# Kernel optimization log

Hardware: AMD Instinct MI355X
Metric: run time of the kernel (lower is better)

## Reference

```python
import jax, jax.numpy as jnp
import numpy as np

B, K, M, L = 16, 256, 16, 64
DET_C, HID, H, DEPTH = 1152, 128, 4, 2
DK = HID // H
SCALE = np.float32(1.0 / np.sqrt(DK))


def _ln(x, g, b):
    mu = jnp.mean(x, -1, keepdims=True)
    v = jnp.mean((x - mu) ** 2, -1, keepdims=True)
    return (x - mu) * jax.lax.rsqrt(v + 1e-5) * g + b


def _bn(x, g, b, m, v):  # eval-mode BatchNorm1d, channel-last
    return (x - m) * (g * jax.lax.rsqrt(v + 1e-5)) + b


def _prelu(x, a):
    return jnp.where(x >= 0, x, a * x)


def _mha(q_in, k_in, v_in, Wq, bq, Wk, bk, Wv, bv, Wo, bo, lg, lb, bias=None, mask=None):
    # MultiHeadAttention: scaled dot-product + residual + LayerNorm (eval, no dropout)
    Bb, Nq, _ = q_in.shape
    Nk = k_in.shape[1]
    q = (q_in @ Wq.T + bq).reshape(Bb, Nq, H, DK).transpose(0, 2, 1, 3)
    k = (k_in @ Wk.T + bk).reshape(Bb, Nk, H, DK).transpose(0, 2, 1, 3)
    v = (v_in @ Wv.T + bv).reshape(Bb, Nk, H, DK).transpose(0, 2, 1, 3)
    att = jnp.einsum('bhqd,bhkd->bhqk', q, k) * SCALE
    if bias is not None:
        att = att + bias  # way='add': per-head distance bias
    if mask is not None:
        att = jnp.where(mask, jnp.float32(-1e9), att)
    att = jax.nn.softmax(att, axis=-1)
    out = jnp.einsum('bhqk,bhkd->bhqd', att, v).transpose(0, 2, 1, 3).reshape(Bb, Nq, HID)
    out = out @ Wo.T + bo
    return _ln(q_in + out, lg, lb)


def setup_inputs() -> dict:
    key = jax.random.key(0)
    ks = iter(jax.random.split(key, 64))
    def nrm(shape, s=0.05):
        return jax.random.normal(next(ks), shape, jnp.float32) * s
    d = {}
    d['center'] = jax.random.normal(next(ks), (B, K, 3), jnp.float32)
    d['detr_features'] = nrm((B, K, DET_C), 1.0)
    d['lang_fea'] = nrm((B * M, L, HID), 1.0)
    d['fc_W1'] = nrm((HID, DET_C)); d['fc_b1'] = jnp.zeros((HID,), jnp.float32)
    for pre in ['bn1', 'mbn1', 'mbn2']:
        d[pre + '_g'] = jnp.ones((HID,), jnp.float32)
        d[pre + '_b'] = jnp.zeros((HID,), jnp.float32)
        d[pre + '_m'] = jnp.zeros((HID,), jnp.float32)
        d[pre + '_v'] = jnp.ones((HID,), jnp.float32)
    d['pr1_a'] = 0.25 * jnp.ones((HID,), jnp.float32)
    d['fc_W2'] = nrm((HID, HID)); d['fc_b2'] = jnp.zeros((HID,), jnp.float32)
    for pre in ['sa', 'ca']:
        for nm in ['Wq', 'Wk', 'Wv', 'Wo']:
            d[f'{pre}_{nm}'] = nrm((DEPTH, HID, HID))
        for nm in ['bq', 'bk', 'bv', 'bo', 'lb']:
            d[f'{pre}_{nm}'] = jnp.zeros((DEPTH, HID), jnp.float32)
        d[f'{pre}_lg'] = jnp.ones((DEPTH, HID), jnp.float32)
    d['m_W1'] = nrm((HID, HID)); d['m_b1'] = jnp.zeros((HID,), jnp.float32)
    d['mp1_a'] = 0.25 * jnp.ones((1,), jnp.float32)
    d['m_W2'] = nrm((HID, HID)); d['m_b2'] = jnp.zeros((HID,), jnp.float32)
    d['mp2_a'] = 0.25 * jnp.ones((1,), jnp.float32)
    d['m_W3'] = nrm((1, HID)); d['m_b3'] = jnp.zeros((1,), jnp.float32)
    d['attention_mask'] = jax.random.bernoulli(next(ks), 0.2, (B * M, 1, 1, L))
    d['len_nun_max'] = M
    return d


def reference(center, detr_features, lang_fea,
              fc_W1, fc_b1, bn1_g, bn1_b, bn1_m, bn1_v, pr1_a, fc_W2, fc_b2,
              sa_Wq, sa_bq, sa_Wk, sa_bk, sa_Wv, sa_bv, sa_Wo, sa_bo, sa_lg, sa_lb,
              ca_Wq, ca_bq, ca_Wk, ca_bk, ca_Wv, ca_bv, ca_Wo, ca_bo, ca_lg, ca_lb,
              m_W1, m_b1, mbn1_g, mbn1_b, mbn1_m, mbn1_v, mp1_a,
              m_W2, m_b2, mbn2_g, mbn2_b, mbn2_m, mbn2_v, mp2_a,
              m_W3, m_b3, attention_mask, len_nun_max):
    # distance-based attention bias (detached in the original)
    c = jax.lax.stop_gradient(center)
    dist = jnp.sqrt(jnp.sum((c[:, None, :, :] - c[:, :, None, :]) ** 2, -1))[:, None]  # (B,1,K,K)
    dw = 1.0 / (dist + 0.01)
    dw = dw / jnp.sum(dw, axis=2, keepdims=True)
    zeros = jnp.zeros_like(dw)
    dist_weights = jnp.concatenate([dw, -dist, zeros, zeros], axis=1)  # (B,H,K,K), one bias per head

    # features_concat: Conv1d(1x1) + BN + PReLU + Conv1d(1x1), channel-last
    x = detr_features @ fc_W1.T + fc_b1
    x = _prelu(_bn(x, bn1_g, bn1_b, bn1_m, bn1_v), pr1_a)
    x = x @ fc_W2.T + fc_b2  # (B,K,HID)

    feats = _mha(x, x, x, sa_Wq[0], sa_bq[0], sa_Wk[0], sa_bk[0], sa_Wv[0], sa_bv[0],
                 sa_Wo[0], sa_bo[0], sa_lg[0], sa_lb[0], bias=dist_weights)

    m = int(len_nun_max)
    feats = jnp.broadcast_to(feats[:, None], (B, m, K, HID)).reshape(B * m, K, HID)
    dwb = jnp.broadcast_to(dist_weights[:, None], (B, m, H, K, K)).reshape(B * m, H, K, K)

    f1 = _mha(feats, lang_fea, lang_fea, ca_Wq[0], ca_bq[0], ca_Wk[0], ca_bk[0], ca_Wv[0],
              ca_bv[0], ca_Wo[0], ca_bo[0], ca_lg[0], ca_lb[0], mask=attention_mask)
    for i in range(1, DEPTH):
        f1 = _mha(f1, f1, f1, sa_Wq[i], sa_bq[i], sa_Wk[i], sa_bk[i], sa_Wv[i], sa_bv[i],
                  sa_Wo[i], sa_bo[i], sa_lg[i], sa_lb[i], bias=dwb)
        f1 = _mha(f1, lang_fea, lang_fea, ca_Wq[i], ca_bq[i], ca_Wk[i], ca_bk[i], ca_Wv[i],
                  ca_bv[i], ca_Wo[i], ca_bo[i], ca_lg[i], ca_lb[i], mask=attention_mask)

    # match head: conv1x1+BN+PReLU x2 + conv1x1 -> 1
    y = f1 @ m_W1.T + m_b1
    y = _prelu(_bn(y, mbn1_g, mbn1_b, mbn1_m, mbn1_v), mp1_a)
    y = y @ m_W2.T + m_b2
    y = _prelu(_bn(y, mbn2_g, mbn2_b, mbn2_m, mbn2_v), mp2_a)
    conf = (y @ m_W3.T + m_b3)[..., 0]  # (B*M, K) cluster_ref
    return conf
```

## Files before the change

kernel.cpp:

```cpp
#include <hip/hip_runtime.h>
#include <hip/hip_bf16.h>
#include <cstdio>

#define KQ   256
#define HID  128
typedef unsigned short u16;
#define SCALE_F 0.1767766952966369f

typedef __bf16 bf16x8 __attribute__((ext_vector_type(8)));
typedef short  s16x8  __attribute__((ext_vector_type(8)));
typedef float  f32x4  __attribute__((ext_vector_type(4)));

static __device__ __forceinline__ float bfu(u16 u) {
    return __uint_as_float(((unsigned)u) << 16);
}
static __device__ __forceinline__ u16 f2b(float f) {
    unsigned u = __float_as_uint(f);
    return (u16)((u + 0x7FFFu + ((u >> 16) & 1u)) >> 16);
}
static __device__ __forceinline__ float ldf(const void* p, int i, int f) {
    return f ? ((const float*)p)[i] : bfu(((const u16*)p)[i]);
}
static __device__ __forceinline__ f32x4 mfma16(s16x8 a, s16x8 b, f32x4 c) {
    return __builtin_amdgcn_mfma_f32_16x16x32_bf16(
        __builtin_bit_cast(bf16x8, a), __builtin_bit_cast(bf16x8, b), c, 0, 0, 0);
}

#define OFF_WB     8256
#define OFF_LANGB  237632
#define OFF_DWB    1286208
#define OFF_DIST   2334784
#define OFF_ROWS   3383360
#define OFF_FEATSB 3387456
#define OFF_FAB    3649600
#define OFF_QB     7843904
#define OFF_KB     12038208
#define OFF_VB     16232512
#define OFF_MASK   20426816
#define NEEDF      20430912

#define WB_FCW1 0
#define WB_FCW2 147456
#define WB_SAWQ 163840
#define WB_SAWK 196608
#define WB_SAWV 229376
#define WB_SAWO 262144
#define WB_CAWQ 294912
#define WB_CAWK 327680
#define WB_CAWV 360448
#define WB_CAWO 393216
#define WB_MW1  425984
#define WB_MW2  442368

__global__ __launch_bounds__(256) void k_detect(
    const unsigned* __restrict__ onesw, const unsigned* __restrict__ maskw,
    int* __restrict__ flags)
{
    __shared__ int fb;
    if (threadIdx.x == 0) fb = 0;
    __syncthreads();
    int any = 0;
    for (int i = threadIdx.x; i < 4096; i += 256) any |= (maskw[i] > 1u) ? 1 : 0;
    if (any) atomicOr(&fb, 1);
    __syncthreads();
    if (threadIdx.x == 0) {
        flags[0] = (onesw[0] == 0x3F800000u) ? 1 : 0;
        flags[1] = fb;
    }
}

__global__ __launch_bounds__(256) void k_mask_canon(
    const unsigned char* __restrict__ raw, const int* __restrict__ flags,
    unsigned char* __restrict__ mask8)
{
    int i = blockIdx.x*256 + threadIdx.x;
    if (flags[1]) mask8[i] = raw[i] ? 1 : 0;
    else          mask8[i] = (((const unsigned int*)raw)[i] != 0u) ? 1 : 0;
}

__global__ __launch_bounds__(256) void k_cv16(
    const void* __restrict__ src, u16* __restrict__ dst, int n,
    const int* __restrict__ flags)
{
    int i = (blockIdx.x*256 + threadIdx.x)*4;
    if (i >= n) return;
    if (flags[0]) {
        float4 v = *(const float4*)((const float*)src + i);
        ushort4 o; o.x = f2b(v.x); o.y = f2b(v.y); o.z = f2b(v.z); o.w = f2b(v.w);
        *(ushort4*)(dst + i) = o;
    } else {
        *(ushort4*)(dst + i) = *(const ushort4*)((const u16*)src + i);
    }
}

__global__ __launch_bounds__(256) void k_dist(
    const void* __restrict__ center, float* __restrict__ dist,
    float* __restrict__ dwraw, float* __restrict__ rowsum,
    const int* __restrict__ flags)
{
    int f  = flags[0];
    int bi = blockIdx.x, b = bi >> 8, j = threadIdx.x;
    float cx = ldf(center, bi*3+0, f), cy = ldf(center, bi*3+1, f), cz = ldf(center, bi*3+2, f);
    int pj = (b << 8) + j;
    float px = ldf(center, pj*3+0, f), py = ldf(center, pj*3+1, f), pz = ldf(center, pj*3+2, f);
    float dx = px-cx, dy = py-cy, dz = pz-cz;
    float d  = sqrtf(dx*dx + dy*dy + dz*dz);
    float w  = 1.f/(d + 0.01f);
    int o = bi*256 + j;
    dist[o]  = d;
    dwraw[o] = w;
    float sw = w;
    #pragma unroll
    for (int m = 32; m >= 1; m >>= 1) sw += __shfl_xor(sw, m);
    __shared__ float red[4];
    if ((j & 63) == 0) red[j >> 6] = sw;
    __syncthreads();
    if (j == 0) rowsum[bi] = red[0] + red[1] + red[2] + red[3];
}

__global__ __launch_bounds__(256) void k_dwnorm(
    float* __restrict__ dw, const float* __restrict__ rowsum)
{
    int i = blockIdx.x*256 + threadIdx.x;
    int b = i >> 16, kc = i & 255;
    dw[i] = dw[i] / rowsum[(b << 8) + kc];
}

template<int EPI, bool ABCAST, bool RBCAST>
__global__ __launch_bounds__(256) void k_gemm(
    const u16* __restrict__ A, const u16* __restrict__ W, u16* __restrict__ C,
    int Kd, const void* __restrict__ bias,
    const void* __restrict__ bng, const void* __restrict__ bnb,
    const void* __restrict__ bnm, const void* __restrict__ bnv,
    const void* __restrict__ pa,
    const void* __restrict__ lg, const void* __restrict__ lb,
    const u16* __restrict__ resid, const int* __restrict__ flags, int voff)
{
    __shared__ __align__(16) u16 Wl[128*136];
    int f = flags[0];
    int t = threadIdx.x, w = t>>6, lane = t&63, lm = lane&15, q4 = lane>>4;
    int m0 = blockIdx.x*64;
    int arow = m0 + w*16 + lm;
    int grow = ABCAST ? (((arow>>12)<<8)|(arow&255)) : arow;
    const u16* Abase = A + (size_t)grow*Kd;
    f32x4 acc[8];
    #pragma unroll
    for (int nt = 0; nt < 8; ++nt) acc[nt] = f32x4{0.f,0.f,0.f,0.f};
    int sr = t>>1, ss = (t&1)*64;
    for (int k0 = 0; k0 < Kd; k0 += 128) {
        const u16* src = W + (size_t)sr*Kd + k0 + ss;
        u16* dst = Wl + sr*136 + ss;
        #pragma unroll
        for (int i = 0; i < 8; ++i) *(s16x8*)(dst + i*8) = *(const s16x8*)(src + i*8);
        __syncthreads();
        s16x8 aF[4];
        #pragma unroll
        for (int ks = 0; ks < 4; ++ks) aF[ks] = *(const s16x8*)(Abase + k0 + ks*32 + q4*8);
        #pragma unroll
        for (int nt = 0; nt < 8; ++nt)
            #pragma unroll
            for (int ks = 0; ks < 4; ++ks) {
                s16x8 bF = *(const s16x8*)(Wl + (nt*16+lm)*136 + ks*32 + q4*8);
                acc[nt] = mfma16(aF[ks], bF, acc[nt]);
            }
        __syncthreads();
    }
    int row = m0 + w*16 + q4*4;
    if (EPI == 3) {
        float xs[8][4];
        #pragma unroll
        for (int nt = 0; nt < 8; ++nt) {
            int ch = nt*16 + lm;
            float bs = ldf(bias, voff + ch, f);
            #pragma unroll
            for (int r = 0; r < 4; ++r) {
                int rr = row + r;
                int rrow = RBCAST ? (((rr>>12)<<8)|(rr&255)) : rr;
                xs[nt][r] = acc[nt][r] + bs + bfu(resid[(size_t)rrow*HID + ch]);
            }
        }
        #pragma unroll
        for (int r = 0; r < 4; ++r) {
            float sm = 0.f, sq = 0.f;
            #pragma unroll
            for (int nt = 0; nt < 8; ++nt) { sm += xs[nt][r]; sq += xs[nt][r]*xs[nt][r]; }
            #pragma unroll
            for (int d = 1; d <= 8; d <<= 1) { sm += __shfl_xor(sm, d); sq += __shfl_xor(sq, d); }
            float mean = sm * (1.f/128.f);
            float var  = sq * (1.f/128.f) - mean*mean;
            float rs   = rsqrtf(var + 1e-5f);
            #pragma unroll
            for (int nt = 0; nt < 8; ++nt) {
                int ch = nt*16 + lm;
                float g = ldf(lg, voff + ch, f), bb = ldf(lb, voff + ch, f);
                C[(size_t)(row+r)*HID + ch] = f2b((xs[nt][r]-mean)*rs*g + bb);
            }
        }
    } else {
        #pragma unroll
        for (int nt = 0; nt < 8; ++nt) {
            int ch = nt*16 + lm;
            float bs = ldf(bias, voff + ch, f);
            float scl = 1.f, sh = 0.f, al = 0.f;
            if (EPI >= 1) {
                float g  = ldf(bng, ch, f), bb = ldf(bnb, ch, f);
                float mn = ldf(bnm, ch, f), vv = ldf(bnv, ch, f);
                scl = g * rsqrtf(vv + 1e-5f);
                sh  = bb - mn*scl;
                al  = (EPI == 2) ? ldf(pa, 0, f) : ldf(pa, ch, f);
            }
            #pragma unroll
            for (int r = 0; r < 4; ++r) {
                float x = acc[nt][r] + bs;
                if (EPI >= 1) { x = x*scl + sh; x = (x >= 0.f) ? x : al*x; }
                C[(size_t)(row+r)*HID + ch] = f2b(x);
            }
        }
    }
}

template<int NK, int MODE>
__global__ __launch_bounds__(256) void k_attn_m(
    const u16* __restrict__ Q, const u16* __restrict__ K, const u16* __restrict__ V,
    u16* __restrict__ O, const float* __restrict__ dwb, const float* __restrict__ dist,
    const unsigned char* __restrict__ mask, int bdiv)
{
    constexpr int NKP = NK + 8;
    __shared__ __align__(16) u16 Vt[32*NKP];
    __shared__ __align__(16) u16 P[4][16*NKP];
    int s = blockIdx.x, h = blockIdx.y, qt = blockIdx.z;
    int t = threadIdx.x, w = t>>6, lane = t&63, lm = lane&15, q4 = lane>>4;
    for (int idx = t; idx < NK*8; idx += 256) {
        int k = idx >> 3, d4 = idx & 7;
        ushort4 u = *(const ushort4*)(V + ((size_t)s*NK + k)*HID + h*32 + d4*4);
        Vt[(d4*4+0)*NKP + k] = u.x;
        Vt[(d4*4+1)*NKP + k] = u.y;
        Vt[(d4*4+2)*NKP + k] = u.z;
        Vt[(d4*4+3)*NKP + k] = u.w;
    }
    __syncthreads();
    int qrow0 = qt*64 + w*16;
    s16x8 aq = *(const s16x8*)(Q + ((size_t)s*KQ + qrow0 + lm)*HID + h*32 + q4*8);
    float S[NK/16][4];
    const float* bp = nullptr; float bsgn = 1.f;
    if (MODE == 1) { if (h == 0) bp = dwb; else if (h == 1) { bp = dist; bsgn = -1.f; } }
    int qb = (MODE == 1) ? ((s/bdiv)*256) : 0;
    #pragma unroll
    for (int kt = 0; kt < NK/16; ++kt) {
        s16x8 bk = *(const s16x8*)(K + ((size_t)s*NK + kt*16 + lm)*HID + h*32 + q4*8);
        f32x4 acc = f32x4{0.f,0.f,0.f,0.f};
        acc = mfma16(aq, bk, acc);
        int key = kt*16 + lm;
        float madd = 0.f;
        if (MODE == 0) madd = mask[s*NK + key] ? -1.0e9f : 0.f;
        #pragma unroll
        for (int r = 0; r < 4; ++r) {
            float sc = acc[r]*SCALE_F;
            if (MODE == 1) { if (bp) sc += bsgn*bp[(size_t)(qb + qrow0 + q4*4 + r)*256 + key]; }
            else sc += madd;
            S[kt][r] = sc;
        }
    }
    float l[4];
    #pragma unroll
    for (int r = 0; r < 4; ++r) {
        float m = -3.0e38f;
        #pragma unroll
        for (int kt = 0; kt < NK/16; ++kt) m = fmaxf(m, S[kt][r]);
        #pragma unroll
        for (int d = 1; d <= 8; d <<= 1) m = fmaxf(m, __shfl_xor(m, d));
        float sum = 0.f;
        #pragma unroll
        for (int kt = 0; kt < NK/16; ++kt) { float p = __expf(S[kt][r]-m); S[kt][r] = p; sum += p; }
        #pragma unroll
        for (int d = 1; d <= 8; d <<= 1) sum += __shfl_xor(sum, d);
        l[r] = sum;
    }
    u16* Pw = P[w];
    #pragma unroll
    for (int kt = 0; kt < NK/16; ++kt)
        #pragma unroll
        for (int r = 0; r < 4; ++r)
            Pw[(q4*4+r)*NKP + kt*16 + lm] = f2b(S[kt][r]);
    __syncthreads();
    #pragma unroll
    for (int nt = 0; nt < 2; ++nt) {
        f32x4 acc = f32x4{0.f,0.f,0.f,0.f};
        #pragma unroll
        for (int ks = 0; ks < NK/32; ++ks) {
            s16x8 ap = *(const s16x8*)(Pw + lm*NKP + ks*32 + q4*8);
            s16x8 bv = *(const s16x8*)(Vt + (nt*16+lm)*NKP + ks*32 + q4*8);
            acc = mfma16(ap, bv, acc);
        }
        #pragma unroll
        for (int r = 0; r < 4; ++r)
            O[((size_t)s*KQ + qrow0 + q4*4 + r)*HID + h*32 + nt*16 + lm] = f2b(acc[r] / l[r]);
    }
}

__global__ __launch_bounds__(256) void k_final(
    const u16* __restrict__ Y, const void* __restrict__ w3,
    const void* __restrict__ b3, void* __restrict__ outp,
    const int* __restrict__ flags)
{
    int f = flags[0];
    int w = threadIdx.x >> 6, lane = threadIdx.x & 63;
    int row = blockIdx.x*4 + w;
    float p = bfu(Y[(size_t)row*HID + lane])*ldf(w3, lane, f)
            + bfu(Y[(size_t)row*HID + 64 + lane])*ldf(w3, 64+lane, f);
    #pragma unroll
    for (int m = 32; m >= 1; m >>= 1) p += __shfl_xor(p, m);
    if (lane == 0) {
        float r = p + ldf(b3, 0, f);
        if (f) ((float*)outp)[row] = r;
        else   ((u16*)outp)[row]   = f2b(r);
    }
}

extern "C" void kernel_launch(void* const* d_in, const int* in_sizes, int n_in,
                              void* d_out, int out_size, void* d_ws, size_t ws_size,
                              hipStream_t stream)
{
    (void)n_in;
    if (ws_size < (size_t)NEEDF * 4) {
        fprintf(stderr, "kernel_launch: ws too small: have %zu need %zu\n",
                ws_size, (size_t)NEEDF * 4);
        hipMemsetAsync(d_out, 0, (size_t)out_size * 2, stream);
        return;
    }
    float* F = (float*)d_ws;
    u16*   U = (u16*)d_ws;
    int* flags = (int*)d_ws;
    u16* WB     = U + (size_t)OFF_WB*2;
    u16* langb  = U + (size_t)OFF_LANGB*2;
    u16* detrb  = U + (size_t)OFF_KB*2;
    u16* featsb = U + (size_t)OFF_FEATSB*2;
    u16* x2b    = U + (size_t)OFF_FAB*2;
    u16* fAb    = U + (size_t)OFF_FAB*2;
    u16* x1b    = U + (size_t)OFF_VB*2;
    u16* Qb     = U + (size_t)OFF_QB*2;
    u16* Kb     = U + (size_t)OFF_KB*2;
    u16* Vb     = U + (size_t)OFF_VB*2;
    float* dwb    = F + OFF_DWB;
    float* dist   = F + OFF_DIST;
    float* rowsum = F + OFF_ROWS;
    unsigned char* mask8 = (unsigned char*)(F + OFF_MASK);

    k_detect<<<1, 256, 0, stream>>>((const unsigned*)d_in[8],
                                    (const unsigned*)d_in[48], flags);
    k_mask_canon<<<64, 256, 0, stream>>>((const unsigned char*)d_in[48], flags, mask8);

    struct { int idx; u16* dst; int n; } cv[14] = {
        {3,  WB+WB_FCW1, 147456}, {18, WB+WB_FCW2, 16384},
        {20, WB+WB_SAWQ, 32768}, {21, WB+WB_SAWK, 32768},
        {22, WB+WB_SAWV, 32768}, {23, WB+WB_SAWO, 32768},
        {30, WB+WB_CAWQ, 32768}, {31, WB+WB_CAWK, 32768},
        {32, WB+WB_CAWV, 32768}, {33, WB+WB_CAWO, 32768},
        {40, WB+WB_MW1, 16384},  {43, WB+WB_MW2, 16384},
        {1,  detrb, 4718592},    {2,  langb, 2097152},
    };
    for (int e = 0; e < 14; ++e)
        k_cv16<<<(cv[e].n + 1023)/1024, 256, 0, stream>>>(
            d_in[cv[e].idx], cv[e].dst, cv[e].n, flags);

    k_dist<<<4096, 256, 0, stream>>>(d_in[0], dist, dwb, rowsum, flags);
    k_dwnorm<<<4096, 256, 0, stream>>>(dwb, rowsum);

    const void* N0 = nullptr;

    k_gemm<1,false,false><<<64, 256, 0, stream>>>(detrb, WB+WB_FCW1, x1b, 1152,
        d_in[4], d_in[5], d_in[6], d_in[7], d_in[8], d_in[17], N0, N0, nullptr, flags, 0);
    k_gemm<0,false,false><<<64, 256, 0, stream>>>(x1b, WB+WB_FCW2, x2b, 128,
        d_in[19], N0,N0,N0,N0,N0, N0, N0, nullptr, flags, 0);

    k_gemm<0,false,false><<<64, 256, 0, stream>>>(x2b, WB+WB_SAWQ, Qb, 128,
        d_in[24], N0,N0,N0,N0,N0, N0, N0, nullptr, flags, 0);
    k_gemm<0,false,false><<<64, 256, 0, stream>>>(x2b, WB+WB_SAWK, Kb, 128,
        d_in[25], N0,N0,N0,N0,N0, N0, N0, nullptr, flags, 0);
    k_gemm<0,false,false><<<64, 256, 0, stream>>>(x2b, WB+WB_SAWV, Vb, 128,
        d_in[26], N0,N0,N0,N0,N0, N0, N0, nullptr, flags, 0);
    k_attn_m<256,1><<<dim3(16,4,4), 256, 0, stream>>>(Qb, Kb, Vb, Qb, dwb, dist, nullptr, 1);
    k_gemm<3,false,false><<<64, 256, 0, stream>>>(Qb, WB+WB_SAWO, featsb, 128,
        d_in[27], N0,N0,N0,N0,N0, d_in[29], d_in[28], x2b, flags, 0);

    k_gemm<0,true, false><<<1024, 256, 0, stream>>>(featsb, WB+WB_CAWQ, Qb, 128,
        d_in[34], N0,N0,N0,N0,N0, N0, N0, nullptr, flags, 0);
    k_gemm<0,false,false><<<256,  256, 0, stream>>>(langb, WB+WB_CAWK, Kb, 128,
        d_in[35], N0,N0,N0,N0,N0, N0, N0, nullptr, flags, 0);
    k_gemm<0,false,false><<<256,  256, 0, stream>>>(langb, WB+WB_CAWV, Vb, 128,
        d_in[36], N0,N0,N0,N0,N0, N0, N0, nullptr, flags, 0);
    k_attn_m<64,0><<<dim3(256,4,4), 256, 0, stream>>>(Qb, Kb, Vb, Qb, nullptr, nullptr, mask8, 1);
    k_gemm<3,false,true><<<1024, 256, 0, stream>>>(Qb, WB+WB_CAWO, fAb, 128,
        d_in[37], N0,N0,N0,N0,N0, d_in[39], d_in[38], featsb, flags, 0);

    k_gemm<0,false,false><<<1024, 256, 0, stream>>>(fAb, WB+WB_SAWQ+16384, Qb, 128,
        d_in[24], N0,N0,N0,N0,N0, N0, N0, nullptr, flags, 128);
    k_gemm<0,false,false><<<1024, 256, 0, stream>>>(fAb, WB+WB_SAWK+16384, Kb, 128,
        d_in[25], N0,N0,N0,N0,N0, N0, N0, nullptr, flags, 128);
    k_gemm<0,false,false><<<1024, 256, 0, stream>>>(fAb, WB+WB_SAWV+16384, Vb, 128,
        d_in[26], N0,N0,N0,N0,N0, N0, N0, nullptr, flags, 128);
    k_attn_m<256,1><<<dim3(256,4,4), 256, 0, stream>>>(Qb, Kb, Vb, Qb, dwb, dist, nullptr, 16);
    k_gemm<3,false,false><<<1024, 256, 0, stream>>>(Qb, WB+WB_SAWO+16384, fAb, 128,
        d_in[27], N0,N0,N0,N0,N0, d_in[29], d_in[28], fAb, flags, 128);

    k_gemm<0,false,false><<<1024, 256, 0, stream>>>(fAb, WB+WB_CAWQ+16384, Qb, 128,
        d_in[34], N0,N0,N0,N0,N0, N0, N0, nullptr, flags, 128);
    k_gemm<0,false,false><<<256,  256, 0, stream>>>(langb, WB+WB_CAWK+16384, Kb, 128,
        d_in[35], N0,N0,N0,N0,N0, N0, N0, nullptr, flags, 128);
    k_gemm<0,false,false><<<256,  256, 0, stream>>>(langb, WB+WB_CAWV+16384, Vb, 128,
        d_in[36], N0,N0,N0,N0,N0, N0, N0, nullptr, flags, 128);
    k_attn_m<64,0><<<dim3(256,4,4), 256, 0, stream>>>(Qb, Kb, Vb, Qb, nullptr, nullptr, mask8, 1);
    k_gemm<3,false,false><<<1024, 256, 0, stream>>>(Qb, WB+WB_CAWO+16384, fAb, 128,
        d_in[37], N0,N0,N0,N0,N0, d_in[39], d_in[38], fAb, flags, 128);

    k_gemm<2,false,false><<<1024, 256, 0, stream>>>(fAb, WB+WB_MW1, Qb, 128,
        d_in[41], d_in[9], d_in[10], d_in[11], d_in[12], d_in[42], N0, N0, nullptr, flags, 0);
    k_gemm<2,false,false><<<1024, 256, 0, stream>>>(Qb, WB+WB_MW2, Kb, 128,
        d_in[44], d_in[13], d_in[14], d_in[15], d_in[16], d_in[45], N0, N0, nullptr, flags, 0);
    k_final<<<16384, 256, 0, stream>>>(Kb, d_in[46], d_in[47], d_out, flags);
}
```

Measured before the change: 622.9 us.

## Recompute distance bias inside self-attention and stage K/V once per head block

Drops the materialised dist and normalized distance-weight matrices and their normalization kernel. Self-attention now recomputes pairwise distances from centers held in shared memory, keeping only a per-row sum buffer. Both attention kernels also loop over the four query tiles inside one block, so K and V for a head are staged in LDS once instead of per query tile. This cuts global traffic for the bias and the repeated K/V loads, at the cost of extra sqrt/div per score for two heads and a quarter as many blocks.

```diff
diff --git a/kernel.cpp b/kernel.cpp
--- a/kernel.cpp
+++ b/kernel.cpp
@@ -93,9 +93,8 @@
     }
 }
 
-__global__ __launch_bounds__(256) void k_dist(
-    const void* __restrict__ center, float* __restrict__ dist,
-    float* __restrict__ dwraw, float* __restrict__ rowsum,
+__global__ __launch_bounds__(256) void k_rowsum(
+    const void* __restrict__ center, float* __restrict__ rowsum,
     const int* __restrict__ flags)
 {
     int f  = flags[0];
@@ -106,9 +105,6 @@
     float dx = px-cx, dy = py-cy, dz = pz-cz;
     float d  = sqrtf(dx*dx + dy*dy + dz*dz);
     float w  = 1.f/(d + 0.01f);
-    int o = bi*256 + j;
-    dist[o]  = d;
-    dwraw[o] = w;
     float sw = w;
     #pragma unroll
     for (int m = 32; m >= 1; m >>= 1) sw += __shfl_xor(sw, m);
@@ -116,14 +112,6 @@
     if ((j & 63) == 0) red[j >> 6] = sw;
     __syncthreads();
     if (j == 0) rowsum[bi] = red[0] + red[1] + red[2] + red[3];
-}
-
-__global__ __launch_bounds__(256) void k_dwnorm(
-    float* __restrict__ dw, const float* __restrict__ rowsum)
-{
-    int i = blockIdx.x*256 + threadIdx.x;
-    int b = i >> 16, kc = i & 255;
-    dw[i] = dw[i] / rowsum[(b << 8) + kc];
 }
 
 template<int EPI, bool ABCAST, bool RBCAST>
@@ -219,82 +207,183 @@
     }
 }
 
-template<int NK, int MODE>
-__global__ __launch_bounds__(256) void k_attn_m(
+__global__ __launch_bounds__(256) void k_sattn(
     const u16* __restrict__ Q, const u16* __restrict__ K, const u16* __restrict__ V,
-    u16* __restrict__ O, const float* __restrict__ dwb, const float* __restrict__ dist,
-    const unsigned char* __restrict__ mask, int bdiv)
-{
-    constexpr int NKP = NK + 8;
-    __shared__ __align__(16) u16 Vt[32*NKP];
-    __shared__ __align__(16) u16 P[4][16*NKP];
-    int s = blockIdx.x, h = blockIdx.y, qt = blockIdx.z;
+    u16* __restrict__ O, const void* __restrict__ center,
+    const float* __restrict__ rowsum, const int* __restrict__ flags, int bdiv)
+{
+    __shared__ __align__(16) u16 Kl[256*40];
+    __shared__ __align__(16) u16 Vt[32*264];
+    __shared__ __align__(16) u16 P[4][16*264];
+    __shared__ float cxl[256], cyl[256], czl[256], rsl[256];
+    int s = blockIdx.x, h = blockIdx.y;
     int t = threadIdx.x, w = t>>6, lane = t&63, lm = lane&15, q4 = lane>>4;
-    for (int idx = t; idx < NK*8; idx += 256) {
+    int f = flags[0];
+    int b = s / bdiv;
+    {
+        const u16* src = K + ((size_t)s*KQ + t)*HID + h*32;
+        u16* dst = Kl + t*40;
+        #pragma unroll
+        for (int i = 0; i < 4; ++i) *(s16x8*)(dst + i*8) = *(const s16x8*)(src + i*8);
+    }
+    for (int idx = t; idx < 256*8; idx += 256) {
         int k = idx >> 3, d4 = idx & 7;
-        ushort4 u = *(const ushort4*)(V + ((size_t)s*NK + k)*HID + h*32 + d4*4);
-        Vt[(d4*4+0)*NKP + k] = u.x;
-        Vt[(d4*4+1)*NKP + k] = u.y;
-        Vt[(d4*4+2)*NKP + k] = u.z;
-        Vt[(d4*4+3)*NKP + k] = u.w;
+        ushort4 u = *(const ushort4*)(V + ((size_t)s*KQ + k)*HID + h*32 + d4*4);
+        Vt[(d4*4+0)*264 + k] = u.x;
+        Vt[(d4*4+1)*264 + k] = u.y;
+        Vt[(d4*4+2)*264 + k] = u.z;
+        Vt[(d4*4+3)*264 + k] = u.w;
+    }
+    {
+        int j = (b << 8) + t;
+        cxl[t] = ldf(center, j*3+0, f);
+        cyl[t] = ldf(center, j*3+1, f);
+        czl[t] = ldf(center, j*3+2, f);
+        rsl[t] = rowsum[j];
     }
     __syncthreads();
-    int qrow0 = qt*64 + w*16;
-    s16x8 aq = *(const s16x8*)(Q + ((size_t)s*KQ + qrow0 + lm)*HID + h*32 + q4*8);
-    float S[NK/16][4];
-    const float* bp = nullptr; float bsgn = 1.f;
-    if (MODE == 1) { if (h == 0) bp = dwb; else if (h == 1) { bp = dist; bsgn = -1.f; } }
-    int qb = (MODE == 1) ? ((s/bdiv)*256) : 0;
-    #pragma unroll
-    for (int kt = 0; kt < NK/16; ++kt) {
-        s16x8 bk = *(const s16x8*)(K + ((size_t)s*NK + kt*16 + lm)*HID + h*32 + q4*8);
-        f32x4 acc = f32x4{0.f,0.f,0.f,0.f};
-        acc = mfma16(aq, bk, acc);
-        int key = kt*16 + lm;
-        float madd = 0.f;
-        if (MODE == 0) madd = mask[s*NK + key] ? -1.0e9f : 0.f;
+    u16* Pw = P[w];
+    for (int qt = 0; qt < 4; ++qt) {
+        int qrow0 = qt*64 + w*16;
+        s16x8 aq = *(const s16x8*)(Q + ((size_t)s*KQ + qrow0 + lm)*HID + h*32 + q4*8);
+        float qx[4], qy[4], qz[4];
+        if (h < 2) {
+            #pragma unroll
+            for (int r = 0; r < 4; ++r) {
+                int q = qrow0 + q4*4 + r;
+                qx[r] = cxl[q]; qy[r] = cyl[q]; qz[r] = czl[q];
+            }
+        }
+        float S[16][4];
+        #pragma unroll
+        for (int kt = 0; kt < 16; ++kt) {
+            s16x8 bF = *(const s16x8*)(Kl + (kt*16+lm)*40 + q4*8);
+            f32x4 acc = f32x4{0.f,0.f,0.f,0.f};
+            acc = mfma16(aq, bF, acc);
+            int key = kt*16 + lm;
+            float kx = 0.f, ky = 0.f, kz = 0.f, rs_ = 1.f;
+            if (h < 2) { kx = cxl[key]; ky = cyl[key]; kz = czl[key]; rs_ = rsl[key]; }
+            #pragma unroll
+            for (int r = 0; r < 4; ++r) {
+                float sc = acc[r]*SCALE_F;
+                if (h < 2) {
+                    float dx = qx[r]-kx, dy = qy[r]-ky, dz = qz[r]-kz;
+                    float d  = sqrtf(dx*dx + dy*dy + dz*dz);
+                    if (h == 0) sc += (1.f/(d + 0.01f)) / rs_;
+                    else        sc -= d;
+                }
+                S[kt][r] = sc;
+            }
+        }
+        float l[4];
         #pragma unroll
         for (int r = 0; r < 4; ++r) {
-            float sc = acc[r]*SCALE_F;
-            if (MODE == 1) { if (bp) sc += bsgn*bp[(size_t)(qb + qrow0 + q4*4 + r)*256 + key]; }
-            else sc += madd;
-            S[kt][r] = sc;
-        }
-    }
-    float l[4];
-    #pragma unroll
-    for (int r = 0; r < 4; ++r) {
-        float m = -3.0e38f;
-        #pragma unroll
-        for (int kt = 0; kt < NK/16; ++kt) m = fmaxf(m, S[kt][r]);
-        #pragma unroll
-        for (int d = 1; d <= 8; d <<= 1) m = fmaxf(m, __shfl_xor(m, d));
-        float sum = 0.f;
-        #pragma unroll
-        for (int kt = 0; kt < NK/16; ++kt) { float p = __expf(S[kt][r]-m); S[kt][r] = p; sum += p; }
-        #pragma unroll
-        for (int d = 1; d <= 8; d <<= 1) sum += __shfl_xor(sum, d);
-        l[r] = sum;
-    }
+            float m = -3.0e38f;
+            #pragma unroll
+            for (int kt = 0; kt < 16; ++kt) m = fmaxf(m, S[kt][r]);
+            #pragma unroll
+            for (int d = 1; d <= 8; d <<= 1) m = fmaxf(m, __shfl_xor(m, d));
+            float sum = 0.f;
+            #pragma unroll
+            for (int kt = 0; kt < 16; ++kt) { float p = __expf(S[kt][r]-m); S[kt][r] = p; sum += p; }
+            #pragma unroll
+            for (int d = 1; d <= 8; d <<= 1) sum += __shfl_xor(sum, d);
+            l[r] = sum;
+        }
+        #pragma unroll
+        for (int kt = 0; kt < 16; ++kt)
+            #pragma unroll
+            for (int r = 0; r < 4; ++r)
+                Pw[(q4*4+r)*264 + kt*16 + lm] = f2b(S[kt][r]);
+        #pragma unroll
+        for (int nt = 0; nt < 2; ++nt) {
+            f32x4 acc = f32x4{0.f,0.f,0.f,0.f};
+            #pragma unroll
+            for (int ks = 0; ks < 8; ++ks) {
+                s16x8 ap = *(const s16x8*)(Pw + lm*264 + ks*32 + q4*8);
+                s16x8 bv = *(const s16x8*)(Vt + (nt*16+lm)*264 + ks*32 + q4*8);
+                acc = mfma16(ap, bv, acc);
+            }
+            #pragma unroll
+            for (int r = 0; r < 4; ++r)
+                O[((size_t)s*KQ + qrow0 + q4*4 + r)*HID + h*32 + nt*16 + lm] = f2b(acc[r] / l[r]);
+        }
+    }
+}
+
+__global__ __launch_bounds__(256) void k_xattn(
+    const u16* __restrict__ Q, const u16* __restrict__ K, const u16* __restrict__ V,
+    u16* __restrict__ O, const unsigned char* __restrict__ mask)
+{
+    __shared__ __align__(16) u16 Kl[64*40];
+    __shared__ __align__(16) u16 Vt[32*72];
+    __shared__ __align__(16) u16 P[4][16*72];
+    __shared__ float madd[64];
+    int s = blockIdx.x, h = blockIdx.y;
+    int t = threadIdx.x, w = t>>6, lane = t&63, lm = lane&15, q4 = lane>>4;
+    if (t < 64) {
+        const u16* src = K + ((size_t)s*64 + t)*HID + h*32;
+        u16* dst = Kl + t*40;
+        #pragma unroll
+        for (int i = 0; i < 4; ++i) *(s16x8*)(dst + i*8) = *(const s16x8*)(src + i*8);
+        madd[t] = mask[s*64 + t] ? -1.0e9f : 0.f;
+    }
+    for (int idx = t; idx < 64*8; idx += 256) {
+        int k = idx >> 3, d4 = idx & 7;
+        ushort4 u = *(const ushort4*)(V + ((size_t)s*64 + k)*HID + h*32 + d4*4);
+        Vt[(d4*4+0)*72 + k] = u.x;
+        Vt[(d4*4+1)*72 + k] = u.y;
+        Vt[(d4*4+2)*72 + k] = u.z;
+        Vt[(d4*4+3)*72 + k] = u.w;
+    }
+    __syncthreads();
     u16* Pw = P[w];
-    #pragma unroll
-    for (int kt = 0; kt < NK/16; ++kt)
-        #pragma unroll
-        for (int r = 0; r < 4; ++r)
-            Pw[(q4*4+r)*NKP + kt*16 + lm] = f2b(S[kt][r]);
-    __syncthreads();
-    #pragma unroll
-    for (int nt = 0; nt < 2; ++nt) {
-        f32x4 acc = f32x4{0.f,0.f,0.f,0.f};
-        #pragma unroll
-        for (int ks = 0; ks < NK/32; ++ks) {
-            s16x8 ap = *(const s16x8*)(Pw + lm*NKP + ks*32 + q4*8);
-            s16x8 bv = *(const s16x8*)(Vt + (nt*16+lm)*NKP + ks*32 + q4*8);
-            acc = mfma16(ap, bv, acc);
-        }
-        #pragma unroll
-        for (int r = 0; r < 4; ++r)
-            O[((size_t)s*KQ + qrow0 + q4*4 + r)*HID + h*32 + nt*16 + lm] = f2b(acc[r] / l[r]);
+    for (int qt = 0; qt < 4; ++qt) {
+        int qrow0 = qt*64 + w*16;
+        s16x8 aq = *(const s16x8*)(Q + ((size_t)s*KQ + qrow0 + lm)*HID + h*32 + q4*8);
+        float S[4][4];
+        #pragma unroll
+        for (int kt = 0; kt < 4; ++kt) {
+            s16x8 bF = *(const s16x8*)(Kl + (kt*16+lm)*40 + q4*8);
+            f32x4 acc = f32x4{0.f,0.f,0.f,0.f};
+            acc = mfma16(aq, bF, acc);
+            float ma = madd[kt*16 + lm];
+            #pragma unroll
+            for (int r = 0; r < 4; ++r) S[kt][r] = acc[r]*SCALE_F + ma;
+        }
+        float l[4];
+        #pragma unroll
+        for (int r = 0; r < 4; ++r) {
+            float m = -3.0e38f;
+            #pragma unroll
+            for (int kt = 0; kt < 4; ++kt) m = fmaxf(m, S[kt][r]);
+            #pragma unroll
+            for (int d = 1; d <= 8; d <<= 1) m = fmaxf(m, __shfl_xor(m, d));
+            float sum = 0.f;
+            #pragma unroll
+            for (int kt = 0; kt < 4; ++kt) { float p = __expf(S[kt][r]-m); S[kt][r] = p; sum += p; }
+            #pragma unroll
+            for (int d = 1; d <= 8; d <<= 1) sum += __shfl_xor(sum, d);
+            l[r] = sum;
+        }
+        #pragma unroll
+        for (int kt = 0; kt < 4; ++kt)
+            #pragma unroll
+            for (int r = 0; r < 4; ++r)
+                Pw[(q4*4+r)*72 + kt*16 + lm] = f2b(S[kt][r]);
+        #pragma unroll
+        for (int nt = 0; nt < 2; ++nt) {
+            f32x4 acc = f32x4{0.f,0.f,0.f,0.f};
+            #pragma unroll
+            for (int ks = 0; ks < 2; ++ks) {
+                s16x8 ap = *(const s16x8*)(Pw + lm*72 + ks*32 + q4*8);
+                s16x8 bv = *(const s16x8*)(Vt + (nt*16+lm)*72 + ks*32 + q4*8);
+                acc = mfma16(ap, bv, acc);
+            }
+            #pragma unroll
+            for (int r = 0; r < 4; ++r)
+                O[((size_t)s*KQ + qrow0 + q4*4 + r)*HID + h*32 + nt*16 + lm] = f2b(acc[r] / l[r]);
+        }
     }
 }
 
@@ -341,8 +430,6 @@
     u16* Qb     = U + (size_t)OFF_QB*2;
     u16* Kb     = U + (size_t)OFF_KB*2;
     u16* Vb     = U + (size_t)OFF_VB*2;
-    float* dwb    = F + OFF_DWB;
-    float* dist   = F + OFF_DIST;
     float* rowsum = F + OFF_ROWS;
     unsigned char* mask8 = (unsigned char*)(F + OFF_MASK);
 
@@ -363,8 +450,7 @@
         k_cv16<<<(cv[e].n + 1023)/1024, 256, 0, stream>>>(
             d_in[cv[e].idx], cv[e].dst, cv[e].n, flags);
 
-    k_dist<<<4096, 256, 0, stream>>>(d_in[0], dist, dwb, rowsum, flags);
-    k_dwnorm<<<4096, 256, 0, stream>>>(dwb, rowsum);
+    k_rowsum<<<4096, 256, 0, stream>>>(d_in[0], rowsum, flags);
 
     const void* N0 = nullptr;
 
@@ -379,7 +465,7 @@
         d_in[25], N0,N0,N0,N0,N0, N0, N0, nullptr, flags, 0);
     k_gemm<0,false,false><<<64, 256, 0, stream>>>(x2b, WB+WB_SAWV, Vb, 128,
         d_in[26], N0,N0,N0,N0,N0, N0, N0, nullptr, flags, 0);
-    k_attn_m<256,1><<<dim3(16,4,4), 256, 0, stream>>>(Qb, Kb, Vb, Qb, dwb, dist, nullptr, 1);
+    k_sattn<<<dim3(16,4), 256, 0, stream>>>(Qb, Kb, Vb, Qb, d_in[0], rowsum, flags, 1);
     k_gemm<3,false,false><<<64, 256, 0, stream>>>(Qb, WB+WB_SAWO, featsb, 128,
         d_in[27], N0,N0,N0,N0,N0, d_in[29], d_in[28], x2b, flags, 0);
 
@@ -389,7 +475,7 @@
         d_in[35], N0,N0,N0,N0,N0, N0, N0, nullptr, flags, 0);
     k_gemm<0,false,false><<<256,  256, 0, stream>>>(langb, WB+WB_CAWV, Vb, 128,
         d_in[36], N0,N0,N0,N0,N0, N0, N0, nullptr, flags, 0);
-    k_attn_m<64,0><<<dim3(256,4,4), 256, 0, stream>>>(Qb, Kb, Vb, Qb, nullptr, nullptr, mask8, 1);
+    k_xattn<<<dim3(256,4), 256, 0, stream>>>(Qb, Kb, Vb, Qb, mask8);
     k_gemm<3,false,true><<<1024, 256, 0, stream>>>(Qb, WB+WB_CAWO, fAb, 128,
         d_in[37], N0,N0,N0,N0,N0, d_in[39], d_in[38], featsb, flags, 0);
 
@@ -399,7 +485,7 @@
         d_in[25], N0,N0,N0,N0,N0, N0, N0, nullptr, flags, 128);
     k_gemm<0,false,false><<<1024, 256, 0, stream>>>(fAb, WB+WB_SAWV+16384, Vb, 128,
         d_in[26], N0,N0,N0,N0,N0, N0, N0, nullptr, flags, 128);
-    k_attn_m<256,1><<<dim3(256,4,4), 256, 0, stream>>>(Qb, Kb, Vb, Qb, dwb, dist, nullptr, 16);
+    k_sattn<<<dim3(256,4), 256, 0, stream>>>(Qb, Kb, Vb, Qb, d_in[0], rowsum, flags, 16);
     k_gemm<3,false,false><<<1024, 256, 0, stream>>>(Qb, WB+WB_SAWO+16384, fAb, 128,
         d_in[27], N0,N0,N0,N0,N0, d_in[29], d_in[28], fAb, flags, 128);
 
@@ -409,7 +495,7 @@
         d_in[35], N0,N0,N0,N0,N0, N0, N0, nullptr, flags, 128);
     k_gemm<0,false,false><<<256,  256, 0, stream>>>(langb, WB+WB_CAWV+16384, Vb, 128,
         d_in[36], N0,N0,N0,N0,N0, N0, N0, nullptr, flags, 128);
-    k_attn_m<64,0><<<dim3(256,4,4), 256, 0, stream>>>(Qb, Kb, Vb, Qb, nullptr, nullptr, mask8, 1);
+    k_xattn<<<dim3(256,4), 256, 0, stream>>>(Qb, Kb, Vb, Qb, mask8);
     k_gemm<3,false,false><<<1024, 256, 0, stream>>>(Qb, WB+WB_CAWO+16384, fAb, 128,
         d_in[37], N0,N0,N0,N0,N0, d_in[39], d_in[38], fAb, flags, 128);
 
```

Result: no change. 614.7 us (-1.3%).
